# Kernel tuning notes

Hardware: AMD Instinct MI355X
Metric: run time of the kernel (lower is better)

The kernel has to match this reference:

```python
import jax, jax.numpy as jnp
import numpy as np

J, L = 4, 8
M = N = 128
B = 2
EPS = 1e-6  # abs_eps smoothing: |z|_eps = sqrt(re^2 + im^2 + eps)


def indices_third_order(J, L):
    # For each bandpass filter i = j1*L + l1, pair with every filter of scale
    # j2 >= j1 (all L angles) plus the lowpass (index J*L).
    # Count = J*L*(L*(J+1)/2 + 1) == num_coefficients.
    i_list, j_list = [], []
    for j1 in range(J):
        for l1 in range(L):
            i = j1 * L + l1
            for j2 in range(j1, J):
                for l2 in range(L):
                    i_list.append(i)
                    j_list.append(j2 * L + l2)
            i_list.append(i)
            j_list.append(J * L)
    return np.asarray(i_list), np.asarray(j_list)


def make_filters(J, L, M, N):
    # Real frequency-domain Morlet-like Gaussian bumps at J scales x L angles,
    # plus one lowpass. Shape (1, J*L+1, M, N), float32.
    kx = 2.0 * np.pi * np.fft.fftfreq(M)[:, None]
    ky = 2.0 * np.pi * np.fft.fftfreq(N)[None, :]
    filts = []
    for j in range(J):
        k0 = 0.8 * np.pi / 2.0 ** j
        sigma = 0.5 * k0
        for l in range(L):
            theta = np.pi * l / L
            cx, cy = k0 * np.cos(theta), k0 * np.sin(theta)
            filts.append(np.exp(-((kx - cx) ** 2 + (ky - cy) ** 2) / (2.0 * sigma ** 2)))
    sigma_lp = 0.8 * np.pi / 2.0 ** J
    filts.append(np.exp(-(kx ** 2 + ky ** 2) / (2.0 * sigma_lp ** 2)))
    return np.stack(filts)[None].astype(np.float32)


def abs_eps(z):
    return jnp.sqrt(z.real ** 2 + z.imag ** 2 + EPS)


def setup_inputs() -> dict:
    key = jax.random.key(0)
    x = jax.random.normal(key, (B, 1, M, N), dtype=jnp.float32)
    filters = jnp.asarray(make_filters(J, L, M, N))  # (1, 33, M, N)
    return {"x": x, "filters": filters}


def reference(x, filters):
    idx0, idx1 = indices_third_order(J, L)
    # first-order filtering: (B, nf, M, N) complex
    xf = jnp.fft.ifft2(filters * jnp.fft.fft2(x))
    xa = abs_eps(xf)  # real (B, nf, M, N)
    # cross-scale correlation: (B, nf_i, nf_j, M, N)
    inner = jnp.fft.ifft2(filters[:, None] * jnp.fft.fft2(xa)[:, :, None])
    out = jnp.real(jnp.conj(xf)[:, None] * inner).mean(axis=(-2, -1))  # (B, nf, nf)
    return out[:, idx0, idx1]  # (B, 672)
```

## Files before the change

### kernel.cpp

```cpp
#include <hip/hip_runtime.h>
#include <math.h>


#define PI_F 3.14159265358979323846f

__device__ __forceinline__ void make_tw(int lane, float* twr, float* twi) {
#pragma unroll
  for (int s = 0; s < 6; ++s) {
    int h = 32 >> s;
    float ang = -PI_F * (float)(lane & (h - 1)) / (float)h;
    float sv, cv;
    __sincosf(ang, &sv, &cv);
    twr[s] = cv; twi[s] = sv;
  }
  float ang = -PI_F * (float)lane / 64.0f;
  float sv, cv;
  __sincosf(ang, &sv, &cv);
  twr[6] = cv; twi[6] = sv;
}

template <int S>
__device__ __forceinline__ void fft128_dif(float& ar, float& ai, float& br, float& bi,
                                           const float* twr, const float* twi, int lane) {
  float s6r = twr[6], s6i = (S > 0) ? twi[6] : -twi[6];
  float ur = ar + br, ui = ai + bi;
  float vr = ar - br, vi = ai - bi;
  ar = ur; ai = ui;
  br = vr * s6r - vi * s6i;
  bi = vr * s6i + vi * s6r;
#pragma unroll
  for (int s = 0; s < 6; ++s) {
    int h = 32 >> s;
    float wr = twr[s], wi = (S > 0) ? twi[s] : -twi[s];
    bool hi = (lane & h) != 0;
    float pr, pi2;
    pr = __shfl_xor(ar, h, 64); pi2 = __shfl_xor(ai, h, 64);
    if (!hi) { ar += pr; ai += pi2; }
    else { float dr = pr - ar, di = pi2 - ai; ar = dr * wr - di * wi; ai = dr * wi + di * wr; }
    pr = __shfl_xor(br, h, 64); pi2 = __shfl_xor(bi, h, 64);
    if (!hi) { br += pr; bi += pi2; }
    else { float dr = pr - br, di = pi2 - bi; br = dr * wr - di * wi; bi = dr * wi + di * wr; }
  }
}

template <int NC>
__device__ __forceinline__ void transpose_r2c_n(float (&dr)[16], float (&di)[16],
    float (&er)[NC], float (&ei)[NC], float (&fr)[NC], float (&fi2)[NC],
    float2 (*tile)[128], int lane, int w, int colbase) {
#pragma unroll
  for (int ch = 0; ch < 2; ++ch) {
    if ((w >> 3) == ch) {
#pragma unroll
      for (int t = 0; t < 8; ++t) {
        int r = w * 8 + t;
        int rr = r & 63, sw = r & 15;
        tile[rr][lane ^ sw] = make_float2(dr[2 * t], di[2 * t]);
        tile[rr][(lane + 64) ^ sw] = make_float2(dr[2 * t + 1], di[2 * t + 1]);
      }
    }
    __syncthreads();
    {
      int sw = lane & 15;
#pragma unroll
      for (int ci = 0; ci < NC; ++ci) {
        int c = colbase + w * NC + ci;
        float2 v = tile[lane][c ^ sw];
        if (ch == 0) { er[ci] = v.x; ei[ci] = v.y; }
        else { fr[ci] = v.x; fi2[ci] = v.y; }
      }
    }
    __syncthreads();
  }
}

__device__ __forceinline__ void make_tw2(int q, float* t2r, float* t2i, float* hw) {
#pragma unroll
  for (int s = 0; s < 5; ++s) {
    int h = 16 >> s;
    float ang = -PI_F * (float)(q & (h - 1)) / (float)h;
    float sv, cv;
    __sincosf(ang, &sv, &cv);
    t2r[s] = cv; t2i[s] = sv;
  }
  float sv, cv;
  __sincosf(-PI_F * (float)q / 64.0f, &sv, &cv);         hw[0] = cv; hw[1] = sv;
  __sincosf(-PI_F * (float)(q + 32) / 64.0f, &sv, &cv);  hw[2] = cv; hw[3] = sv;
  __sincosf(-PI_F * (float)q / 32.0f, &sv, &cv);         hw[4] = cv; hw[5] = sv;
}

template <int S>
__device__ __forceinline__ void fft128x2_dif(float (&cr)[4], float (&ci)[4],
    const float* t2r, const float* t2i, const float* hw, int q) {
  float T0r = hw[0], T0i = (S > 0) ? hw[1] : -hw[1];
  float T1r = hw[2], T1i = (S > 0) ? hw[3] : -hw[3];
  float T2r = hw[4], T2i = (S > 0) ? hw[5] : -hw[5];
  {
    float ur = cr[0] + cr[2], ui = ci[0] + ci[2];
    float vr = cr[0] - cr[2], vi = ci[0] - ci[2];
    cr[0] = ur; ci[0] = ui;
    cr[2] = vr * T0r - vi * T0i; ci[2] = vr * T0i + vi * T0r;
    ur = cr[1] + cr[3]; ui = ci[1] + ci[3];
    vr = cr[1] - cr[3]; vi = ci[1] - ci[3];
    cr[1] = ur; ci[1] = ui;
    cr[3] = vr * T1r - vi * T1i; ci[3] = vr * T1i + vi * T1r;
  }
  {
    float ur = cr[0] + cr[1], ui = ci[0] + ci[1];
    float vr = cr[0] - cr[1], vi = ci[0] - ci[1];
    cr[0] = ur; ci[0] = ui;
    cr[1] = vr * T2r - vi * T2i; ci[1] = vr * T2i + vi * T2r;
    ur = cr[2] + cr[3]; ui = ci[2] + ci[3];
    vr = cr[2] - cr[3]; vi = ci[2] - ci[3];
    cr[2] = ur; ci[2] = ui;
    cr[3] = vr * T2r - vi * T2i; ci[3] = vr * T2i + vi * T2r;
  }
#pragma unroll
  for (int s = 0; s < 5; ++s) {
    int h = 16 >> s;
    float wr = t2r[s], wi = (S > 0) ? t2i[s] : -t2i[s];
    bool hi = (q & h) != 0;
#pragma unroll
    for (int m = 0; m < 4; ++m) {
      float pr = __shfl_xor(cr[m], h, 64);
      float pi2 = __shfl_xor(ci[m], h, 64);
      if (!hi) { cr[m] += pr; ci[m] += pi2; }
      else { float dr = pr - cr[m], di = pi2 - ci[m];
             cr[m] = dr * wr - di * wi; ci[m] = dr * wi + di * wr; }
    }
  }
}

__global__ __launch_bounds__(1024, 2) void k_prep(const float* __restrict__ x,
    float2* __restrict__ X, float* __restrict__ out, const float* __restrict__ F,
    float* __restrict__ G) {
  __shared__ float2 tile[64][128];
  int tid = threadIdx.x;
  int bx = blockIdx.x;
  if (bx == 8) {
    if (tid < 1344) out[tid] = 0.f;
    return;
  }
  if (bx >= 9) {
    int q = bx - 9;
    int j = q >> 2, part = q & 3;
    const float* Fj = F + j * 16384;
    float* Gj = G + j * 16384;
#pragma unroll
    for (int it = 0; it < 4; ++it) {
      int k = part * 4096 + it * 1024 + tid;
      int u = k >> 7, v = k & 127;
      int un = (128 - u) & 127, vn = (128 - v) & 127;
      float f = Fj[k], fn = Fj[un * 128 + vn];
      Gj[k] = 0.5f * (f * f + fn * fn);
    }
    return;
  }
  int b = bx >> 2, quarter = bx & 3;
  int lane = tid & 63, w = tid >> 6;
  float twr[7], twi[7]; make_tw(lane, twr, twi);
  const float* xb = x + b * 16384;
  float dr[16], di[16];
  float er[2], ei[2], fr[2], fi2[2];
#pragma unroll
  for (int t = 0; t < 8; ++t) {
    int r = w * 8 + t;
    float ar = xb[r * 128 + lane], ai2 = 0.f, br = xb[r * 128 + lane + 64], bi = 0.f;
    fft128_dif<1>(ar, ai2, br, bi, twr, twi, lane);
    dr[2 * t] = ar; di[2 * t] = ai2; dr[2 * t + 1] = br; di[2 * t + 1] = bi;
  }
  transpose_r2c_n<2>(dr, di, er, ei, fr, fi2, tile, lane, w, quarter * 32);
  int u0 = __brev((unsigned)lane) >> 25;
#pragma unroll
  for (int ci = 0; ci < 2; ++ci) {
    int c = quarter * 32 + w * 2 + ci;
    float ar = er[ci], ai2 = ei[ci], br = fr[ci], bi = fi2[ci];
    fft128_dif<1>(ar, ai2, br, bi, twr, twi, lane);
    int vn = __brev((unsigned)c) >> 25;
    X[b * 16384 + u0 * 128 + vn] = make_float2(ar, ai2);
    X[b * 16384 + (u0 + 1) * 128 + vn] = make_float2(br, bi);
  }
}

__global__ __launch_bounds__(1024, 1) void k_fields(const float2* __restrict__ X,
    const float* __restrict__ F, const float* __restrict__ G,
    float* __restrict__ dfld, float* __restrict__ xa) {
  __shared__ float2 tile[64][128];
  int tid = threadIdx.x, lane = tid & 63, w = tid >> 6;
  int g = lane >> 5, q = lane & 31;
  int bx = blockIdx.x;
  bool isd = (bx < 68);
  int b, half;
  bool has1 = false;
  const float* g0 = nullptr; const float* g1 = nullptr; const float* Fb = nullptr;
  float* o0; float* o1 = nullptr;
  if (isd) {
    int dp = bx >> 1; half = bx & 1;
    b = dp / 17; int p = dp - b * 17;
    int j0 = 2 * p; has1 = (p < 16);
    g0 = G + j0 * 16384;
    g1 = G + (j0 + 1) * 16384;
    o0 = dfld + (b * 33 + j0) * 16384;
    o1 = dfld + (b * 33 + j0 + 1) * 16384;
  } else {
    int qq = bx - 68; int qi = qq >> 1; half = qq & 1;
    b = qi >> 5; int f = qi & 31;
    Fb = F + f * 16384;
    o0 = xa + qi * 16384;
  }
  float t2r[5], t2i[5], hw[6];
  make_tw2(q, t2r, t2i, hw);
  const float2* Xb = X + b * 16384;

  float sr[4][4], si[4][4];
#pragma unroll
  for (int k = 0; k < 4; ++k) {
    int r = w * 8 + 2 * k + g;
    float cr[4], ci[4];
#pragma unroll
    for (int m = 0; m < 4; ++m) {
      int p = q + 32 * m;
      float2 xv = Xb[r * 128 + p];
      if (isd) {
        float ga = g0[r * 128 + p];
        float gb = has1 ? g1[r * 128 + p] : 0.f;
        cr[m] = xv.x * ga - xv.y * gb; ci[m] = xv.y * ga + xv.x * gb;
      } else {
        float f0 = Fb[r * 128 + p];
        cr[m] = xv.x * f0; ci[m] = xv.y * f0;
      }
    }
    fft128x2_dif<-1>(cr, ci, t2r, t2i, hw, q);
#pragma unroll
    for (int m = 0; m < 4; ++m) { sr[k][m] = cr[m]; si[k][m] = ci[m]; }
  }

  float pr[2][4], pi2a[2][4];
  int colbase = half * 64;
#pragma unroll
  for (int ch = 0; ch < 2; ++ch) {
    if ((w >> 3) == ch) {
#pragma unroll
      for (int k = 0; k < 4; ++k) {
        int r = w * 8 + 2 * k + g;
        int rr = r & 63, sw = r & 15;
#pragma unroll
        for (int m = 0; m < 4; ++m)
          tile[rr][(32 * m + q) ^ sw] = make_float2(sr[k][m], si[k][m]);
      }
    }
    __syncthreads();
    {
      int sw = q & 15;
#pragma unroll
      for (int j = 0; j < 2; ++j) {
        int c = colbase + w * 4 + 2 * j + g;
#pragma unroll
        for (int mm = 0; mm < 2; ++mm) {
          float2 v = tile[32 * mm + q][c ^ sw];
          pr[j][2 * ch + mm] = v.x; pi2a[j][2 * ch + mm] = v.y;
        }
      }
    }
    __syncthreads();
  }

  const float sc = 1.0f / 16384.0f;
#pragma unroll
  for (int j = 0; j < 2; ++j) {
    fft128x2_dif<-1>(pr[j], pi2a[j], t2r, t2i, hw, q);
    int c = colbase + w * 4 + 2 * j + g;
#pragma unroll
    for (int m = 0; m < 4; ++m) {
      int su = 32 * m + q;
      if (isd) {
        o0[c * 128 + su] = pr[j][m];
        if (has1) o1[c * 128 + su] = pi2a[j][m];
      } else {
        float tr = pr[j][m] * sc, ti = pi2a[j][m] * sc;
        o0[c * 128 + su] = sqrtf(tr * tr + ti * ti + 1e-6f);
      }
    }
  }
}

__global__ __launch_bounds__(512) void k_dot(const float* __restrict__ xa,
    const float* __restrict__ dfld, float* __restrict__ out) {
  int qb = blockIdx.x;
  int im = qb >> 3;
  int slice = (qb >> 1) & 3;
  int jh = qb & 1;
  int b = im >> 5, i = im & 31;
  int j0 = jh * 17;
  int t = threadIdx.x;
  const float4* xr = (const float4*)(xa + im * 16384 + slice * 4096);
  const float4* db = (const float4*)(dfld + (b * 33 + j0) * 16384 + slice * 4096);
  float acc[17];
#pragma unroll
  for (int j = 0; j < 17; ++j) acc[j] = 0.f;
#pragma unroll
  for (int it = 0; it < 2; ++it) {
    int k = it * 512 + t;
    float4 xv = xr[k];
#pragma unroll
    for (int j = 0; j < 17; ++j) {
      float4 dv = db[j * 4096 + k];
      acc[j] += xv.x * dv.x + xv.y * dv.y + xv.z * dv.z + xv.w * dv.w;
    }
  }
#pragma unroll
  for (int j = 0; j < 17; ++j) {
#pragma unroll
    for (int off = 32; off > 0; off >>= 1) acc[j] += __shfl_xor(acc[j], off, 64);
  }
  __shared__ float red[8][17];
  int w = t >> 6, lane = t & 63;
  if (lane == 0) {
#pragma unroll
    for (int j = 0; j < 17; ++j) red[w][j] = acc[j];
  }
  __syncthreads();
  if (t < 17) {
    int j = j0 + t;
    float s = 0.f;
#pragma unroll
    for (int w2 = 0; w2 < 8; ++w2) s += red[w2][t];
    int j1 = i >> 3, l1 = i & 7;
    const int pref[4] = {0, 264, 464, 600};
    int per = (4 - j1) * 8 + 1;
    int start = pref[j1] + l1 * per;
    int pos = -1;
    if (j == 32) pos = start + per - 1;
    else if (j < 32) {
      int j2 = j >> 3;
      if (j2 >= j1) pos = start + (j2 - j1) * 8 + (j & 7);
    }
    if (pos >= 0)
      atomicAdd(out + b * 672 + pos, s * (1.0f / 16384.0f) * (1.0f / 16384.0f));
  }
}

extern "C" void kernel_launch(void* const* d_in, const int* in_sizes, int n_in,
                              void* d_out, int out_size, void* d_ws, size_t ws_size,
                              hipStream_t stream) {
  (void)in_sizes; (void)n_in; (void)out_size; (void)ws_size;
  const float* x = (const float*)d_in[0];
  const float* F = (const float*)d_in[1];
  float* out = (float*)d_out;
  char* ws = (char*)d_ws;
  float2* X = (float2*)(ws + 0);
  float* dfld = (float*)(ws + 262144);
  float* xa = (float*)(ws + 4587520);
  float* G = (float*)(ws + 8781824);

  hipLaunchKernelGGL(k_prep, dim3(141), dim3(1024), 0, stream, x, X, out, F, G);
  hipLaunchKernelGGL(k_fields, dim3(196), dim3(1024), 0, stream, X, F, G, dfld, xa);
  hipLaunchKernelGGL(k_dot, dim3(512), dim3(512), 0, stream, xa, dfld, out);
}
```

Baseline: 103.5 us.

## Pack real rows into complex FFTs, drop trivial last-stage twiddles, split k_dot finer

The first row FFT pass in k_prep now packs two real rows into one complex FFT and separates them with a Hermitian-symmetry shuffle step, halving row FFT work. The last butterfly stage in both FFT routines skips the twiddle multiply, since its twiddle is always 1. k_dot is split into four j-groups of 9 instead of two of 17, doubling the grid to lower per-thread register use and raise parallelism. The cost is some redundant j-range coverage (36 slots for 33 filters), which needs bounds handling, plus extra cross-lane shuffles.

New measurement: 96.73 us. -6.5%, faster.

```diff
diff --git a/kernel.cpp b/kernel.cpp
--- a/kernel.cpp
+++ b/kernel.cpp
@@ -29,7 +29,7 @@
   br = vr * s6r - vi * s6i;
   bi = vr * s6i + vi * s6r;
 #pragma unroll
-  for (int s = 0; s < 6; ++s) {
+  for (int s = 0; s < 5; ++s) {
     int h = 32 >> s;
     float wr = twr[s], wi = (S > 0) ? twi[s] : -twi[s];
     bool hi = (lane & h) != 0;
@@ -40,6 +40,14 @@
     pr = __shfl_xor(br, h, 64); pi2 = __shfl_xor(bi, h, 64);
     if (!hi) { br += pr; bi += pi2; }
     else { float dr = pr - br, di = pi2 - bi; br = dr * wr - di * wi; bi = dr * wi + di * wr; }
+  }
+  {
+    bool hi = (lane & 1) != 0;
+    float pr, pi2;
+    pr = __shfl_xor(ar, 1, 64); pi2 = __shfl_xor(ai, 1, 64);
+    if (!hi) { ar += pr; ai += pi2; } else { ar = pr - ar; ai = pi2 - ai; }
+    pr = __shfl_xor(br, 1, 64); pi2 = __shfl_xor(bi, 1, 64);
+    if (!hi) { br += pr; bi += pi2; } else { br = pr - br; bi = pi2 - bi; }
   }
 }
 
@@ -115,7 +123,7 @@
     cr[3] = vr * T2r - vi * T2i; ci[3] = vr * T2i + vi * T2r;
   }
 #pragma unroll
-  for (int s = 0; s < 5; ++s) {
+  for (int s = 0; s < 4; ++s) {
     int h = 16 >> s;
     float wr = t2r[s], wi = (S > 0) ? t2i[s] : -t2i[s];
     bool hi = (q & h) != 0;
@@ -126,6 +134,16 @@
       if (!hi) { cr[m] += pr; ci[m] += pi2; }
       else { float dr = pr - cr[m], di = pi2 - ci[m];
              cr[m] = dr * wr - di * wi; ci[m] = dr * wi + di * wr; }
+    }
+  }
+  {
+    bool hi = (q & 1) != 0;
+#pragma unroll
+    for (int m = 0; m < 4; ++m) {
+      float pr = __shfl_xor(cr[m], 1, 64);
+      float pi2 = __shfl_xor(ci[m], 1, 64);
+      if (!hi) { cr[m] += pr; ci[m] += pi2; }
+      else { cr[m] = pr - cr[m]; ci[m] = pi2 - ci[m]; }
     }
   }
 }
@@ -159,17 +177,35 @@
   int lane = tid & 63, w = tid >> 6;
   float twr[7], twi[7]; make_tw(lane, twr, twi);
   const float* xb = x + b * 16384;
+  int u0 = __brev((unsigned)lane) >> 25;
+  int spA = __brev((unsigned)((128 - u0) & 127)) >> 25;
+  int spB = __brev((unsigned)(127 - u0)) >> 25;
   float dr[16], di[16];
   float er[2], ei[2], fr[2], fi2[2];
 #pragma unroll
-  for (int t = 0; t < 8; ++t) {
-    int r = w * 8 + t;
-    float ar = xb[r * 128 + lane], ai2 = 0.f, br = xb[r * 128 + lane + 64], bi = 0.f;
+  for (int t = 0; t < 4; ++t) {
+    int r0 = w * 8 + 2 * t;
+    float ar = xb[r0 * 128 + lane],      ai2 = xb[(r0 + 1) * 128 + lane];
+    float br = xb[r0 * 128 + lane + 64], bi  = xb[(r0 + 1) * 128 + lane + 64];
     fft128_dif<1>(ar, ai2, br, bi, twr, twi, lane);
-    dr[2 * t] = ar; di[2 * t] = ai2; dr[2 * t + 1] = br; di[2 * t + 1] = bi;
+    int la = spA & 63;
+    float fAr = __shfl(ar, la, 64), fAi = __shfl(ai2, la, 64);
+    float fBr = __shfl(br, la, 64), fBi = __shfl(bi, la, 64);
+    float Pr = (spA < 64) ? fAr : fBr, Pi = (spA < 64) ? fAi : fBi;
+    float X0r = 0.5f * (ar + Pr),  X0i = 0.5f * (ai2 - Pi);
+    float X1r = 0.5f * (ai2 + Pi), X1i = 0.5f * (Pr - ar);
+    int lb = spB & 63;
+    float gAr = __shfl(ar, lb, 64), gAi = __shfl(ai2, lb, 64);
+    float gBr = __shfl(br, lb, 64), gBi = __shfl(bi, lb, 64);
+    float Qr = (spB < 64) ? gAr : gBr, Qi = (spB < 64) ? gAi : gBi;
+    float Y0r = 0.5f * (br + Qr), Y0i = 0.5f * (bi - Qi);
+    float Y1r = 0.5f * (bi + Qi), Y1i = 0.5f * (Qr - br);
+    dr[2 * (2 * t)] = X0r;     di[2 * (2 * t)] = X0i;
+    dr[2 * (2 * t) + 1] = Y0r; di[2 * (2 * t) + 1] = Y0i;
+    dr[2 * (2 * t + 1)] = X1r;     di[2 * (2 * t + 1)] = X1i;
+    dr[2 * (2 * t + 1) + 1] = Y1r; di[2 * (2 * t + 1) + 1] = Y1i;
   }
   transpose_r2c_n<2>(dr, di, er, ei, fr, fi2, tile, lane, w, quarter * 32);
-  int u0 = __brev((unsigned)lane) >> 25;
 #pragma unroll
   for (int ci = 0; ci < 2; ++ci) {
     int c = quarter * 32 + w * 2 + ci;
@@ -286,40 +322,40 @@
 __global__ __launch_bounds__(512) void k_dot(const float* __restrict__ xa,
     const float* __restrict__ dfld, float* __restrict__ out) {
   int qb = blockIdx.x;
-  int im = qb >> 3;
-  int slice = (qb >> 1) & 3;
-  int jh = qb & 1;
+  int im = qb >> 4;
+  int slice = (qb >> 2) & 3;
+  int jq = qb & 3;
   int b = im >> 5, i = im & 31;
-  int j0 = jh * 17;
+  int j0 = jq * 9;
   int t = threadIdx.x;
   const float4* xr = (const float4*)(xa + im * 16384 + slice * 4096);
   const float4* db = (const float4*)(dfld + (b * 33 + j0) * 16384 + slice * 4096);
-  float acc[17];
-#pragma unroll
-  for (int j = 0; j < 17; ++j) acc[j] = 0.f;
+  float acc[9];
+#pragma unroll
+  for (int j = 0; j < 9; ++j) acc[j] = 0.f;
 #pragma unroll
   for (int it = 0; it < 2; ++it) {
     int k = it * 512 + t;
     float4 xv = xr[k];
 #pragma unroll
-    for (int j = 0; j < 17; ++j) {
+    for (int j = 0; j < 9; ++j) {
       float4 dv = db[j * 4096 + k];
       acc[j] += xv.x * dv.x + xv.y * dv.y + xv.z * dv.z + xv.w * dv.w;
     }
   }
 #pragma unroll
-  for (int j = 0; j < 17; ++j) {
+  for (int j = 0; j < 9; ++j) {
 #pragma unroll
     for (int off = 32; off > 0; off >>= 1) acc[j] += __shfl_xor(acc[j], off, 64);
   }
-  __shared__ float red[8][17];
+  __shared__ float red[8][9];
   int w = t >> 6, lane = t & 63;
   if (lane == 0) {
 #pragma unroll
-    for (int j = 0; j < 17; ++j) red[w][j] = acc[j];
+    for (int j = 0; j < 9; ++j) red[w][j] = acc[j];
   }
   __syncthreads();
-  if (t < 17) {
+  if (t < 9) {
     int j = j0 + t;
     float s = 0.f;
 #pragma unroll
@@ -354,5 +390,5 @@
 
   hipLaunchKernelGGL(k_prep, dim3(141), dim3(1024), 0, stream, x, X, out, F, G);
   hipLaunchKernelGGL(k_fields, dim3(196), dim3(1024), 0, stream, X, F, G, dfld, xa);
-  hipLaunchKernelGGL(k_dot, dim3(512), dim3(512), 0, stream, xa, dfld, out);
-}
+  hipLaunchKernelGGL(k_dot, dim3(1024), dim3(512), 0, stream, xa, dfld, out);
+}
```
